# Kernel optimization log

Measured on AMD Instinct MI355X. Metric: run time of the kernel, lower is better.

## Reference

```python
import jax, jax.numpy as jnp
import numpy as np

VOCAB = 50257
EMB = 256
HID = 512
BATCH = 32
SEQ = 512
PAD_ID = 0


def setup_inputs() -> dict:
    key = jax.random.key(0)
    k1, k2, k3, k4, k5, k6 = jax.random.split(key, 6)
    input_ids = jax.random.randint(k1, (BATCH, SEQ), 0, VOCAB, dtype=jnp.int32)
    attention_mask = jax.random.randint(k2, (BATCH, SEQ), 0, 2, dtype=jnp.int32)
    # learned params
    embed_table = jax.random.normal(k3, (VOCAB, EMB), dtype=jnp.float32) * 0.02
    Wx = jax.random.normal(k4, (EMB, HID), dtype=jnp.float32) / np.sqrt(EMB)
    Wh = jax.random.normal(k5, (HID, HID), dtype=jnp.float32) / np.sqrt(HID)
    b = jnp.zeros((HID,), dtype=jnp.float32)
    return {"input_ids": input_ids, "attention_mask": attention_mask,
            "embed_table": embed_table, "Wx": Wx, "Wh": Wh, "b": b}


def reference(input_ids, attention_mask, embed_table, Wx, Wh, b):
    # Embedding lookup: [B, S, E]
    emb = embed_table[input_ids]
    # time-major for scan: [S, B, E] and [S, B]
    xs = jnp.swapaxes(emb, 0, 1)
    ms = jnp.swapaxes(attention_mask, 0, 1)
    h0 = jnp.zeros((emb.shape[0], Wh.shape[0]), dtype=emb.dtype)

    def step(h, xm):
        x_t, m_t = xm  # [B, E], [B]
        h_new = jnp.tanh(x_t @ Wx + h @ Wh + b)  # Elman RNN cell
        h_next = jnp.where((m_t != PAD_ID)[:, None], h_new, h)
        return h_next, h_next

    final_h, all_h_tmajor = jax.lax.scan(step, h0, (xs, ms))
    all_h = jnp.swapaxes(all_h_tmajor, 0, 1)  # [B, S, H]
    return all_h, final_h
```

## Files before the change

kernel.cpp:

```cpp
#include <hip/hip_runtime.h>

#define VOCAB 50257
#define EMB 256
#define HID 512
#define BATCH 32
#define SEQ 512

typedef _Float16 h2 __attribute__((ext_vector_type(2)));
typedef unsigned int u32;

#if __has_builtin(__builtin_amdgcn_fdot2)
#define FDOT2(a, b, c) __builtin_amdgcn_fdot2((a), (b), (c), false)
#else
static __device__ __forceinline__ float FDOT2(h2 a, h2 b, float c) {
    return c + (float)a.x * (float)b.x + (float)a.y * (float)b.y;
}
#endif

static __device__ __forceinline__ h2 mk2(float a, float b) {
    h2 r; r.x = (_Float16)a; r.y = (_Float16)b; return r;
}
static __device__ __forceinline__ u32 pk_rtn(float a, float b) {
    return __builtin_bit_cast(u32, mk2(a, b));
}
static __device__ __forceinline__ h2 as_h2(u32 v) {
    return __builtin_bit_cast(h2, v);
}

__global__ __launch_bounds__(256) void xprec_kernel(
    const int* __restrict__ ids, const float* __restrict__ emb,
    const float* __restrict__ Wx, const float* __restrict__ bias,
    float* __restrict__ allh)
{
    __shared__ float embL[32][EMB];
    const int tid  = threadIdx.x;
    const int tok0 = blockIdx.x * 32;

    {
        const int t    = tid >> 3;
        const int part = tid & 7;
        const int id   = ids[tok0 + t];
        const float4* src = (const float4*)(emb + (size_t)id * EMB + part * 32);
        float4* dst = (float4*)(&embL[t][part * 32]);
#pragma unroll
        for (int k = 0; k < 8; ++k) dst[k] = src[k];
    }
    __syncthreads();

    const int j0 = tid * 2;
    float2 acc[32];
    const float2 bv = *(const float2*)(bias + j0);
#pragma unroll
    for (int t = 0; t < 32; ++t) acc[t] = bv;

    for (int e = 0; e < EMB; e += 4) {
        const float2 w0 = *(const float2*)(Wx + (size_t)(e + 0) * HID + j0);
        const float2 w1 = *(const float2*)(Wx + (size_t)(e + 1) * HID + j0);
        const float2 w2 = *(const float2*)(Wx + (size_t)(e + 2) * HID + j0);
        const float2 w3 = *(const float2*)(Wx + (size_t)(e + 3) * HID + j0);
#pragma unroll
        for (int t = 0; t < 32; ++t) {
            const float4 ev = *(const float4*)(&embL[t][e]);
            acc[t].x += ev.x * w0.x + ev.y * w1.x + ev.z * w2.x + ev.w * w3.x;
            acc[t].y += ev.x * w0.y + ev.y * w1.y + ev.z * w2.y + ev.w * w3.y;
        }
    }

#pragma unroll
    for (int t = 0; t < 32; ++t) {
        *(float2*)(allh + (size_t)(tok0 + t) * HID + j0) = acc[t];
    }
}

__global__ __launch_bounds__(512, 2) void rnn_local_kernel(
    const int* __restrict__ mask, const float* __restrict__ Wh,
    float* __restrict__ allh, float* __restrict__ finalh)
{
    __shared__ uint4 wl[2][8][512];
    __shared__ float zp[8][8][64];
    __shared__ int   mlist[SEQ];
    __shared__ int   nmL;

    const int tid = threadIdx.x;
    const int b   = blockIdx.x;
    const int c   = tid & 63;
    const int p   = tid >> 6;

    int* maskL = (int*)zp;
    maskL[tid] = mask[b * SEQ + tid];
    __syncthreads();
    if (tid == 0) {
        int n = 0;
        for (int t = 0; t < SEQ; ++t) if (maskL[t]) mlist[n++] = t;
        nmL = n;
    }

    const float* wb = Wh + (size_t)(64 * p) * HID + c;
    h2 wv0[32], wv1[32], wv2[32], wv3[32], wv4[32], wv5[32];
#pragma unroll
    for (int i = 0; i < 32; ++i) {
        const float* r0 = wb + (size_t)(2 * i) * HID;
        const float* r1 = r0 + HID;
        wv0[i] = mk2(r0[0 * 64], r1[0 * 64]);
        wv1[i] = mk2(r0[1 * 64], r1[1 * 64]);
        wv2[i] = mk2(r0[2 * 64], r1[2 * 64]);
        wv3[i] = mk2(r0[3 * 64], r1[3 * 64]);
        wv4[i] = mk2(r0[4 * 64], r1[4 * 64]);
        wv5[i] = mk2(r0[5 * 64], r1[5 * 64]);
    }
#pragma unroll
    for (int blk = 0; blk < 8; ++blk) {
        uint4 v6, v7;
        u32* v6p = (u32*)&v6; u32* v7p = (u32*)&v7;
#pragma unroll
        for (int e = 0; e < 4; ++e) {
            const float* r0 = wb + (size_t)(blk * 8 + 2 * e) * HID;
            const float* r1 = r0 + HID;
            v6p[e] = pk_rtn(r0[6 * 64], r1[6 * 64]);
            v7p[e] = pk_rtn(r0[7 * 64], r1[7 * 64]);
        }
        wl[0][blk][tid] = v6;
        wl[1][blk][tid] = v7;
    }
    __syncthreads();
    const int nm = nmL;

    float* arow = allh + (size_t)b * SEQ * HID;

    {
        const int end0 = nm ? mlist[0] : SEQ;
        for (int t = 0; t < end0; ++t) arow[(size_t)t * HID + tid] = 0.f;
    }

    u32 hs[32];
#pragma unroll
    for (int i = 0; i < 32; ++i) hs[i] = 0u;

    float hreg  = 0.f;
    float xnext = 0.f;
    if (nm) xnext = arow[(size_t)mlist[0] * HID + tid];

    for (int it = 0; it < nm; ++it) {
        const int t    = mlist[it];
        const int tend = (it + 1 < nm) ? mlist[it + 1] : SEQ;
        const float x  = xnext;
        if (it + 1 < nm)
            xnext = arow[(size_t)mlist[it + 1] * HID + tid];

        float a0 = 0.f, a1 = 0.f, a2 = 0.f, a3 = 0.f;
        float a4 = 0.f, a5 = 0.f, a6 = 0.f, a7 = 0.f;
#pragma unroll
        for (int blk = 0; blk < 8; ++blk) {
            const uint4 w6 = wl[0][blk][tid];
            const uint4 w7 = wl[1][blk][tid];
            const u32* w6p = (const u32*)&w6;
            const u32* w7p = (const u32*)&w7;
#pragma unroll
            for (int e = 0; e < 4; ++e) {
                const int i = blk * 4 + e;
                const h2 hv = as_h2(hs[i]);
                a0 = FDOT2(wv0[i], hv, a0);
                a1 = FDOT2(wv1[i], hv, a1);
                a2 = FDOT2(wv2[i], hv, a2);
                a3 = FDOT2(wv3[i], hv, a3);
                a4 = FDOT2(wv4[i], hv, a4);
                a5 = FDOT2(wv5[i], hv, a5);
                a6 = FDOT2(as_h2(w6p[e]), hv, a6);
                a7 = FDOT2(as_h2(w7p[e]), hv, a7);
            }
        }
        zp[p][0][c] = a0; zp[p][1][c] = a1; zp[p][2][c] = a2; zp[p][3][c] = a3;
        zp[p][4][c] = a4; zp[p][5][c] = a5; zp[p][6][c] = a6; zp[p][7][c] = a7;
        __syncthreads();

        const float z = zp[0][p][c] + zp[1][p][c] + zp[2][p][c] + zp[3][p][c]
                      + zp[4][p][c] + zp[5][p][c] + zp[6][p][c] + zp[7][p][c];
        const float hn = tanhf(x + z);
        hreg = hn;
        for (int tt = t; tt < tend; ++tt)
            arow[(size_t)tt * HID + tid] = hn;

        const float hpartner = __shfl_xor(hn, 1);
        const u32 pku = pk_rtn(hn, hpartner);
#pragma unroll
        for (int i = 0; i < 32; ++i)
            hs[i] = (u32)__builtin_amdgcn_readlane((int)pku, 2 * i);

        __syncthreads();
    }
    finalh[b * HID + tid] = hreg;
}

extern "C" void kernel_launch(void* const* d_in, const int* in_sizes, int n_in,
                              void* d_out, int out_size, void* d_ws, size_t ws_size,
                              hipStream_t stream) {
    const int*   ids  = (const int*)d_in[0];
    const int*   msk  = (const int*)d_in[1];
    const float* emb  = (const float*)d_in[2];
    const float* Wx   = (const float*)d_in[3];
    const float* Wh   = (const float*)d_in[4];
    const float* bias = (const float*)d_in[5];

    float* allh   = (float*)d_out;
    float* finalh = (float*)d_out + (size_t)BATCH * SEQ * HID;

    xprec_kernel<<<BATCH * SEQ / 32, 256, 0, stream>>>(ids, emb, Wx, bias, allh);
    rnn_local_kernel<<<BATCH, 512, 0, stream>>>(msk, Wh, allh, finalh);
}
```

Baseline: 694.0 us.

## Halve RNN block to 256 threads, each computing two hidden units

The recurrent kernel now runs 256 threads per batch row instead of 512. Each wavefront covers 128 rows of Wh in registers and LDS, and each thread produces two hidden outputs. The new h vector is shared through an fp16 LDS buffer and broadcast with readlane inside the dot-product loop, rather than unpacked into 32 registers after a shuffle. This is meant to cut barrier cost and the cross-wave partial-sum reduction on each serial timestep, in exchange for twice the register-resident weights per thread (spill risk) and less latency hiding with one wave per SIMD.

```diff
diff --git a/kernel.cpp b/kernel.cpp
--- a/kernel.cpp
+++ b/kernel.cpp
@@ -72,14 +72,15 @@
     }
 }
 
-__global__ __launch_bounds__(512, 2) void rnn_local_kernel(
+__global__ __launch_bounds__(256, 1) void rnn_local_kernel(
     const int* __restrict__ mask, const float* __restrict__ Wh,
     float* __restrict__ allh, float* __restrict__ finalh)
 {
-    __shared__ uint4 wl[2][8][512];
-    __shared__ float zp[8][8][64];
-    __shared__ int   mlist[SEQ];
-    __shared__ int   nmL;
+    __shared__ uint4    wl[2][16][256];
+    __shared__ float    zp[4][8][64];
+    __shared__ _Float16 hF[HID];
+    __shared__ int      mlist[SEQ];
+    __shared__ int      nmL;
 
     const int tid = threadIdx.x;
     const int b   = blockIdx.x;
@@ -87,7 +88,8 @@
     const int p   = tid >> 6;
 
     int* maskL = (int*)zp;
-    maskL[tid] = mask[b * SEQ + tid];
+    maskL[tid]       = mask[b * SEQ + tid];
+    maskL[tid + 256] = mask[b * SEQ + tid + 256];
     __syncthreads();
     if (tid == 0) {
         int n = 0;
@@ -95,32 +97,32 @@
         nmL = n;
     }
 
-    const float* wb = Wh + (size_t)(64 * p) * HID + c;
-    h2 wv0[32], wv1[32], wv2[32], wv3[32], wv4[32], wv5[32];
-#pragma unroll
-    for (int i = 0; i < 32; ++i) {
+    const float* wb = Wh + (size_t)(128 * p) * HID + c;
+    h2 w0[64], w1[64], w2[64], w3[64], w4[64], w5[64];
+#pragma unroll
+    for (int i = 0; i < 64; ++i) {
         const float* r0 = wb + (size_t)(2 * i) * HID;
         const float* r1 = r0 + HID;
-        wv0[i] = mk2(r0[0 * 64], r1[0 * 64]);
-        wv1[i] = mk2(r0[1 * 64], r1[1 * 64]);
-        wv2[i] = mk2(r0[2 * 64], r1[2 * 64]);
-        wv3[i] = mk2(r0[3 * 64], r1[3 * 64]);
-        wv4[i] = mk2(r0[4 * 64], r1[4 * 64]);
-        wv5[i] = mk2(r0[5 * 64], r1[5 * 64]);
-    }
-#pragma unroll
-    for (int blk = 0; blk < 8; ++blk) {
+        w0[i] = mk2(r0[0 * 64], r1[0 * 64]);
+        w1[i] = mk2(r0[1 * 64], r1[1 * 64]);
+        w2[i] = mk2(r0[2 * 64], r1[2 * 64]);
+        w3[i] = mk2(r0[3 * 64], r1[3 * 64]);
+        w4[i] = mk2(r0[4 * 64], r1[4 * 64]);
+        w5[i] = mk2(r0[5 * 64], r1[5 * 64]);
+    }
+#pragma unroll
+    for (int i4 = 0; i4 < 16; ++i4) {
         uint4 v6, v7;
         u32* v6p = (u32*)&v6; u32* v7p = (u32*)&v7;
 #pragma unroll
         for (int e = 0; e < 4; ++e) {
-            const float* r0 = wb + (size_t)(blk * 8 + 2 * e) * HID;
+            const float* r0 = wb + (size_t)(8 * i4 + 2 * e) * HID;
             const float* r1 = r0 + HID;
             v6p[e] = pk_rtn(r0[6 * 64], r1[6 * 64]);
             v7p[e] = pk_rtn(r0[7 * 64], r1[7 * 64]);
         }
-        wl[0][blk][tid] = v6;
-        wl[1][blk][tid] = v7;
+        wl[0][i4][tid] = v6;
+        wl[1][i4][tid] = v7;
     }
     __syncthreads();
     const int nm = nmL;
@@ -129,42 +131,48 @@
 
     {
         const int end0 = nm ? mlist[0] : SEQ;
-        for (int t = 0; t < end0; ++t) arow[(size_t)t * HID + tid] = 0.f;
-    }
-
-    u32 hs[32];
-#pragma unroll
-    for (int i = 0; i < 32; ++i) hs[i] = 0u;
-
-    float hreg  = 0.f;
-    float xnext = 0.f;
-    if (nm) xnext = arow[(size_t)mlist[0] * HID + tid];
+        for (int t = 0; t < end0; ++t) {
+            arow[(size_t)t * HID + tid]       = 0.f;
+            arow[(size_t)t * HID + tid + 256] = 0.f;
+        }
+    }
+
+    u32   hpk = 0u;
+    float hr1 = 0.f, hr2 = 0.f;
+    float x1n = 0.f, x2n = 0.f;
+    if (nm) {
+        x1n = arow[(size_t)mlist[0] * HID + tid];
+        x2n = arow[(size_t)mlist[0] * HID + tid + 256];
+    }
 
     for (int it = 0; it < nm; ++it) {
         const int t    = mlist[it];
         const int tend = (it + 1 < nm) ? mlist[it + 1] : SEQ;
-        const float x  = xnext;
-        if (it + 1 < nm)
-            xnext = arow[(size_t)mlist[it + 1] * HID + tid];
+        const float x1 = x1n, x2 = x2n;
+        if (it + 1 < nm) {
+            x1n = arow[(size_t)mlist[it + 1] * HID + tid];
+            x2n = arow[(size_t)mlist[it + 1] * HID + tid + 256];
+        }
 
         float a0 = 0.f, a1 = 0.f, a2 = 0.f, a3 = 0.f;
         float a4 = 0.f, a5 = 0.f, a6 = 0.f, a7 = 0.f;
 #pragma unroll
-        for (int blk = 0; blk < 8; ++blk) {
-            const uint4 w6 = wl[0][blk][tid];
-            const uint4 w7 = wl[1][blk][tid];
+        for (int i4 = 0; i4 < 16; ++i4) {
+            const uint4 w6 = wl[0][i4][tid];
+            const uint4 w7 = wl[1][i4][tid];
             const u32* w6p = (const u32*)&w6;
             const u32* w7p = (const u32*)&w7;
 #pragma unroll
             for (int e = 0; e < 4; ++e) {
-                const int i = blk * 4 + e;
-                const h2 hv = as_h2(hs[i]);
-                a0 = FDOT2(wv0[i], hv, a0);
-                a1 = FDOT2(wv1[i], hv, a1);
-                a2 = FDOT2(wv2[i], hv, a2);
-                a3 = FDOT2(wv3[i], hv, a3);
-                a4 = FDOT2(wv4[i], hv, a4);
-                a5 = FDOT2(wv5[i], hv, a5);
+                const int i = i4 * 4 + e;
+                const u32 hu = (u32)__builtin_amdgcn_readlane((int)hpk, i);
+                const h2  hv = as_h2(hu);
+                a0 = FDOT2(w0[i], hv, a0);
+                a1 = FDOT2(w1[i], hv, a1);
+                a2 = FDOT2(w2[i], hv, a2);
+                a3 = FDOT2(w3[i], hv, a3);
+                a4 = FDOT2(w4[i], hv, a4);
+                a5 = FDOT2(w5[i], hv, a5);
                 a6 = FDOT2(as_h2(w6p[e]), hv, a6);
                 a7 = FDOT2(as_h2(w7p[e]), hv, a7);
             }
@@ -173,22 +181,23 @@
         zp[p][4][c] = a4; zp[p][5][c] = a5; zp[p][6][c] = a6; zp[p][7][c] = a7;
         __syncthreads();
 
-        const float z = zp[0][p][c] + zp[1][p][c] + zp[2][p][c] + zp[3][p][c]
-                      + zp[4][p][c] + zp[5][p][c] + zp[6][p][c] + zp[7][p][c];
-        const float hn = tanhf(x + z);
-        hreg = hn;
-        for (int tt = t; tt < tend; ++tt)
-            arow[(size_t)tt * HID + tid] = hn;
-
-        const float hpartner = __shfl_xor(hn, 1);
-        const u32 pku = pk_rtn(hn, hpartner);
-#pragma unroll
-        for (int i = 0; i < 32; ++i)
-            hs[i] = (u32)__builtin_amdgcn_readlane((int)pku, 2 * i);
-
+        const float z1 = zp[0][p][c] + zp[1][p][c] + zp[2][p][c] + zp[3][p][c];
+        const float z2 = zp[0][p + 4][c] + zp[1][p + 4][c]
+                       + zp[2][p + 4][c] + zp[3][p + 4][c];
+        const float h1 = tanhf(x1 + z1);
+        const float hh2 = tanhf(x2 + z2);
+        hr1 = h1; hr2 = hh2;
+        hF[tid]       = (_Float16)h1;
+        hF[tid + 256] = (_Float16)hh2;
+        for (int tt = t; tt < tend; ++tt) {
+            arow[(size_t)tt * HID + tid]       = h1;
+            arow[(size_t)tt * HID + tid + 256] = hh2;
+        }
         __syncthreads();
-    }
-    finalh[b * HID + tid] = hreg;
+        hpk = ((const u32*)hF)[64 * p + c];
+    }
+    finalh[b * HID + tid]       = hr1;
+    finalh[b * HID + tid + 256] = hr2;
 }
 
 extern "C" void kernel_launch(void* const* d_in, const int* in_sizes, int n_in,
@@ -205,5 +214,5 @@
     float* finalh = (float*)d_out + (size_t)BATCH * SEQ * HID;
 
     xprec_kernel<<<BATCH * SEQ / 32, 256, 0, stream>>>(ids, emb, Wx, bias, allh);
-    rnn_local_kernel<<<BATCH, 512, 0, stream>>>(msk, Wh, allh, finalh);
-}
+    rnn_local_kernel<<<BATCH, 256, 0, stream>>>(msk, Wh, allh, finalh);
+}
```

Result: slower. 0.9998 ms (+44.1%).
